# Performance work log

Hardware: AMD Instinct MI355X
Metric: run time of the kernel (lower is better)

The kernel has to match this reference:

```python
import jax, jax.numpy as jnp
import numpy as np

D = 64; H = 6; DH = 32; CB = 16; SB = 8; NSEL = 2; WIN = 7; OUT = 7; HID = 32
SCALE = DH ** -0.5
NEG = -3.4e38  # max_neg_value for fp32 masking


def _rope(x):
    # interleaved (lucidrains rotary-embedding-torch style), theta=10000
    n, d = x.shape[-2], x.shape[-1]
    inv = 1.0 / (10000.0 ** (jnp.arange(0, d, 2, dtype=jnp.float32) / d))
    fr = jnp.arange(n, dtype=jnp.float32)[:, None] * inv[None, :]  # n, d/2
    fr = jnp.repeat(fr, 2, axis=-1)                                # n, d
    c, s = jnp.cos(fr), jnp.sin(fr)
    xr = jnp.stack((-x[..., 1::2], x[..., 0::2]), axis=-1).reshape(x.shape)
    return x * c + xr * s


def reference(x, We, be, gamma, Wq, Wk, Wv, k_pos, v_pos, mem_k, mem_v,
              Wkc1, bkc1, Wkc2, bkc2, Wvc1, bvc1, Wvc2, bvc2,
              Wg, bg, Wo, Wh1, bh1, Wh2, bh2):
    B, N = x.shape
    nC = N // CB  # compressed blocks
    nF = N // SB  # fine/selection blocks

    # per-feature scalar embedding: Linear(1, 64)
    h = x[..., None] * We[0] + be  # B,N,D

    # RMSNorm (F.normalize * sqrt(D) * (gamma + 1))
    nrm = jnp.sqrt(jnp.sum(h * h, axis=-1, keepdims=True))
    hn = h / jnp.maximum(nrm, 1e-12) * jnp.sqrt(float(D)) * (gamma + 1.0)

    def proj(W):
        return jnp.einsum('bnd,de->bne', hn, W).reshape(B, N, H, DH).transpose(0, 2, 1, 3)
    q, k, v = proj(Wq), proj(Wk), proj(Wv)  # B,H,N,DH

    # ---- compressed branch (un-rotated q,k; intra-block pos emb + MLP compressor) ----
    kp = jnp.tile(k_pos, (1, nC, 1))  # H,N,DH
    vp = jnp.tile(v_pos, (1, nC, 1))
    CD = CB * DH
    kc_in = (k + kp).reshape(B, H, nC, CD)
    vc_in = (v + vp).reshape(B, H, nC, CD)
    ck = jax.nn.relu(kc_in @ Wkc1 + bkc1) @ Wkc2 + bkc2  # B,H,nC,DH
    cv = jax.nn.relu(vc_in @ Wvc1 + bvc1) @ Wvc2 + bvc2
    ck = jnp.concatenate([jnp.broadcast_to(mem_k, (B, H, 1, DH)), ck], axis=2)
    cv = jnp.concatenate([jnp.broadcast_to(mem_v, (B, H, 1, DH)), cv], axis=2)
    csim = jnp.einsum('bhid,bhjd->bhij', q, ck) * SCALE  # B,H,N,1+nC
    ck_last = jnp.concatenate([jnp.array([-1]), (jnp.arange(nC) + 1) * CB - 1])
    cmask = ck_last[None, :] < jnp.arange(N)[:, None]    # causal: block fully in past (mem kv always visible)
    csim = jnp.where(cmask, csim, NEG)
    c_out = jnp.einsum('bhij,bhjd->bhid', jax.nn.softmax(csim, axis=-1), cv)

    # ---- importance scores -> top-k selection blocks ----
    # compress_block_size != selection_block_size: repeat compressed scores, block-causal mask,
    # mean-pool to selection granularity (uniform within block -> direct mapping), pad+softmax
    rep = CB // SB
    imp = csim[..., 1:][..., jnp.arange(nF) // rep]  # B,H,N,nF
    qb = jnp.arange(N) // SB
    imp = jnp.where(qb[:, None] > jnp.arange(nF)[None, :], imp, NEG)  # strictly-past blocks only
    imp = jnp.concatenate([jnp.full(imp.shape[:-1] + (1,), -1e3, imp.dtype), imp], axis=-1)
    p = jax.nn.softmax(imp, axis=-1)[..., 1:]
    vals, idx = jax.lax.top_k(p, NSEL)  # B,H,N,NSEL

    # rotary only for fine + sliding branches
    qr, kr = _rope(q), _rope(k)

    # ---- fine (selected-block) branch ----
    sel = jnp.concatenate([idx, jnp.broadcast_to(qb[None, None, :, None], (B, H, N, 1))], axis=-1)  # own block appended
    kb = kr.reshape(B, H, nF, SB, DH)
    vb = v.reshape(B, H, nF, SB, DH)
    bi = jnp.arange(B)[:, None, None, None]
    hi = jnp.arange(H)[None, :, None, None]
    fk = kb[bi, hi, sel].reshape(B, H, N, (NSEL + 1) * SB, DH)
    fv = vb[bi, hi, sel].reshape(B, H, N, (NSEL + 1) * SB, DH)
    fmask_sel = jnp.repeat(vals > 1e-10, SB, axis=-1)                     # B,H,N,NSEL*SB
    own = jnp.arange(SB)[None, :] <= (jnp.arange(N) % SB)[:, None]        # causal within own block
    fmask = jnp.concatenate([fmask_sel, jnp.broadcast_to(own, (B, H, N, SB))], axis=-1)
    fsim = jnp.einsum('bhid,bhijd->bhij', qr, fk) * SCALE
    fsim = jnp.where(fmask, fsim, NEG)
    f_out = jnp.einsum('bhij,bhijd->bhid', jax.nn.softmax(fsim, axis=-1), fv)

    off = jnp.arange(WIN + 1)
    kidx = jnp.arange(N)[:, None] - off[None, :]
    valid = kidx >= 0
    kidx = jnp.maximum(kidx, 0)
    sk = kr[:, :, kidx]
    sv = v[:, :, kidx]
    ssim = jnp.einsum('bhid,bhiwd->bhiw', qr, sk) * SCALE
    ssim = jnp.where(valid, ssim, NEG)
    s_out = jnp.einsum('bhiw,bhiwd->bhid', jax.nn.softmax(ssim, axis=-1), sv)

    # ---- sigmoid-gated strategy combine (order: compressed, fine, sliding) ----
    g = jax.nn.sigmoid(jnp.einsum('bnd,de->bne', hn, Wg) + bg).reshape(B, N, H, 3).transpose(0, 2, 1, 3)
    out = g[..., 0:1] * c_out + g[..., 1:2] * f_out + g[..., 2:3] * s_out  # B,H,N,DH
    out = out.transpose(0, 2, 1, 3).reshape(B, N, H * DH) @ Wo             # B,N,D

    # model head: mean-pool over features, MLP
    pooled = out.mean(axis=1)
    hh = jax.nn.gelu(pooled @ Wh1 + bh1, approximate=False)
    return hh @ Wh2 + bh2


def setup_inputs() -> dict:
    key = jax.random.key(0)
    ks = jax.random.split(key, 20)
    B, N = 32, 512
    CD = CB * DH
    f32 = jnp.float32

    def rn(k, shape, fan_in):
        return jax.random.normal(k, shape, f32) / np.sqrt(fan_in)

    return {
        'x': jax.random.normal(ks[0], (B, N), f32),
        'We': rn(ks[1], (1, D), 1),
        'be': jnp.zeros((D,), f32),
        'gamma': 0.1 * jax.random.normal(ks[2], (D,), f32),
        'Wq': rn(ks[3], (D, H * DH), D),
        'Wk': rn(ks[4], (D, H * DH), D),
        'Wv': rn(ks[5], (D, H * DH), D),
        'k_pos': 0.02 * jax.random.normal(ks[6], (H, CB, DH), f32),
        'v_pos': 0.02 * jax.random.normal(ks[7], (H, CB, DH), f32),
        'mem_k': 0.02 * jax.random.normal(ks[8], (H, 1, DH), f32),
        'mem_v': 0.02 * jax.random.normal(ks[9], (H, 1, DH), f32),
        'Wkc1': rn(ks[10], (CD, CD), CD), 'bkc1': jnp.zeros((CD,), f32),
        'Wkc2': rn(ks[11], (CD, DH), CD), 'bkc2': jnp.zeros((DH,), f32),
        'Wvc1': rn(ks[12], (CD, CD), CD), 'bvc1': jnp.zeros((CD,), f32),
        'Wvc2': rn(ks[13], (CD, DH), CD), 'bvc2': jnp.zeros((DH,), f32),
        'Wg': rn(ks[14], (D, 3 * H), D),
        'bg': jnp.tile(jnp.array([-2.0, -2.0, 2.0], f32), H),
        'Wo': rn(ks[15], (H * DH, D), H * DH),
        'Wh1': rn(ks[16], (D, HID), D), 'bh1': jnp.zeros((HID,), f32),
        'Wh2': rn(ks[17], (HID, OUT), HID), 'bh2': jnp.zeros((OUT,), f32),
    }
```

## Files before the change

### kernel.cpp

```cpp
#include <hip/hip_runtime.h>

typedef unsigned short ushort_t;
typedef __attribute__((ext_vector_type(8))) short bf16x8;
typedef __attribute__((ext_vector_type(4))) float f32x4;

constexpr int N_   = 512;
constexpr int D_   = 64;
constexpr int H_   = 6;
constexpr int DH_  = 32;
constexpr int CB_  = 16;
constexpr int SB_  = 8;
constexpr int HD_  = H_ * DH_;
constexpr int CD_  = CB_ * DH_;
constexpr int nC_  = N_ / CB_;
constexpr int nF_  = N_ / SB_;
constexpr float SCALE_ = 0.17677669529663687f;
constexpr float NEG_ = -3.4e38f;

__device__ __forceinline__ ushort_t f2bf(float x) {
    unsigned u = __float_as_uint(x);
    unsigned r = u + 0x7FFFu + ((u >> 16) & 1u);
    return (ushort_t)(r >> 16);
}

__device__ __forceinline__ size_t frag_addr(int row, int k) {
    return (size_t)(row >> 4) * 8192 + (size_t)(k >> 5) * 512
         + (size_t)((k >> 3) & 3) * 128 + (size_t)(row & 15) * 8 + (k & 7);
}

__global__ __launch_bounds__(256) void k_cvtW(
    const float* __restrict__ Wk1, const float* __restrict__ Wv1,
    ushort_t* __restrict__ wtk_hi, ushort_t* __restrict__ wtk_lo,
    ushort_t* __restrict__ wtv_hi, ushort_t* __restrict__ wtv_lo)
{
    const float* W = blockIdx.z ? Wv1 : Wk1;
    ushort_t* ohi = blockIdx.z ? wtv_hi : wtk_hi;
    ushort_t* olo = blockIdx.z ? wtv_lo : wtk_lo;
    const int k0 = blockIdx.x * 64, j0 = blockIdx.y * 64;
    const int t = threadIdx.x;
    __shared__ float tile[64][65];
    #pragma unroll 4
    for (int i = 0; i < 16; ++i) {
        const int lin = t + i * 256;
        const int kk = lin >> 6, jj = lin & 63;
        tile[kk][jj] = W[(size_t)(k0 + kk) * 512 + j0 + jj];
    }
    __syncthreads();
    #pragma unroll 4
    for (int i = 0; i < 16; ++i) {
        const int lin = t + i * 256;
        const int jj = lin >> 6, kk = lin & 63;
        const float x = tile[kk][jj];
        const ushort_t h = f2bf(x);
        const float hf = __uint_as_float((unsigned)h << 16);
        const size_t fo = frag_addr(j0 + jj, k0 + kk);
        ohi[fo] = h;
        olo[fo] = f2bf(x - hf);
    }
}

__global__ __launch_bounds__(192) void k_embed(
    const float* __restrict__ x, const float* __restrict__ We, const float* __restrict__ be,
    const float* __restrict__ gamma,
    const float* __restrict__ Wq, const float* __restrict__ Wk, const float* __restrict__ Wv,
    const float* __restrict__ kpos, const float* __restrict__ vpos,
    const float* __restrict__ Wg, const float* __restrict__ bg,
    float* __restrict__ q, float* __restrict__ qr, float* __restrict__ kr,
    float* __restrict__ v,
    ushort_t* __restrict__ kin_hi, ushort_t* __restrict__ kin_lo,
    ushort_t* __restrict__ vin_hi, ushort_t* __restrict__ vin_lo,
    float* __restrict__ g)
{
    const int t  = threadIdx.x;
    const int wv = t >> 6;
    const int ln = t & 63;
    const int n00 = blockIdx.x * 16;
    const int b = n00 / N_;
    const int nbase = n00 % N_;

    __shared__ float hn[16][64];

    for (int r = wv; r < 16; r += 3) {
        const int n = nbase + r;
        float xv = x[b * N_ + n];
        float h = fmaf(xv, We[ln], be[ln]);
        float ss = h * h;
        #pragma unroll
        for (int off = 32; off; off >>= 1) ss += __shfl_down(ss, off);
        ss = __shfl(ss, 0);
        float sc = 8.0f / fmaxf(sqrtf(ss), 1e-12f);
        hn[r][ln] = h * sc * (gamma[ln] + 1.0f);
    }
    __syncthreads();

    const int e  = ln + (wv << 6);
    const int hh = e >> 5;
    const int dh = e & 31;
    float aq[16], ak[16], av[16];
    #pragma unroll
    for (int r = 0; r < 16; ++r) { aq[r] = 0.f; ak[r] = 0.f; av[r] = 0.f; }
    for (int dd = 0; dd < 64; dd += 4) {
        float wq4[4], wk4[4], wv4[4];
        #pragma unroll
        for (int u = 0; u < 4; ++u) {
            wq4[u] = Wq[(dd + u) * HD_ + e];
            wk4[u] = Wk[(dd + u) * HD_ + e];
            wv4[u] = Wv[(dd + u) * HD_ + e];
        }
        #pragma unroll
        for (int r = 0; r < 16; ++r) {
            const float4 hv = *(const float4*)&hn[r][dd];
            aq[r] = fmaf(hv.x, wq4[0], aq[r]);
            aq[r] = fmaf(hv.y, wq4[1], aq[r]);
            aq[r] = fmaf(hv.z, wq4[2], aq[r]);
            aq[r] = fmaf(hv.w, wq4[3], aq[r]);
            ak[r] = fmaf(hv.x, wk4[0], ak[r]);
            ak[r] = fmaf(hv.y, wk4[1], ak[r]);
            ak[r] = fmaf(hv.z, wk4[2], ak[r]);
            ak[r] = fmaf(hv.w, wk4[3], ak[r]);
            av[r] = fmaf(hv.x, wv4[0], av[r]);
            av[r] = fmaf(hv.y, wv4[1], av[r]);
            av[r] = fmaf(hv.z, wv4[2], av[r]);
            av[r] = fmaf(hv.w, wv4[3], av[r]);
        }
    }
    const float invf = exp2f((float)(dh & ~1) * -0.41524101186092029f);
    #pragma unroll
    for (int r = 0; r < 16; ++r) {
        const int n = nbase + r;
        const size_t o = ((size_t)(b * H_ + hh) * N_ + n) * DH_ + dh;
        q[o] = aq[r];
        v[o] = av[r];
        const int pix = (hh * CB_ + (n & (CB_ - 1))) * DH_ + dh;
        const float kinv = ak[r] + kpos[pix];
        const float vinv = av[r] + vpos[pix];
        {
            const int row = (b * H_ + hh) * nC_ + (n >> 4);
            const int k   = (n & 15) * 32 + dh;
            const size_t fo = frag_addr(row, k);
            const ushort_t kh = f2bf(kinv);
            kin_hi[fo] = kh;
            kin_lo[fo] = f2bf(kinv - __uint_as_float((unsigned)kh << 16));
            const ushort_t vh = f2bf(vinv);
            vin_hi[fo] = vh;
            vin_lo[fo] = f2bf(vinv - __uint_as_float((unsigned)vh << 16));
        }
        const float aqp = __shfl_xor(aq[r], 1);
        const float akp = __shfl_xor(ak[r], 1);
        float sA, cA;
        __sincosf((float)n * invf, &sA, &cA);
        float rq, rk;
        if (dh & 1) { rq = fmaf(aqp, sA, aq[r] * cA); rk = fmaf(akp, sA, ak[r] * cA); }
        else        { rq = fmaf(-aqp, sA, aq[r] * cA); rk = fmaf(-akp, sA, ak[r] * cA); }
        qr[o] = rq; kr[o] = rk;
    }

    if (ln < 18) {
        for (int r = wv; r < 16; r += 3) {
            const int n = nbase + r;
            float a = bg[ln];
            for (int dd = 0; dd < 64; ++dd) a = fmaf(hn[r][dd], Wg[dd * 18 + ln], a);
            const float gv = 1.0f / (1.0f + __expf(-a));
            g[((size_t)(b * H_ + ln / 3) * N_ + n) * 3 + (ln % 3)] = gv;
        }
    }
}

__global__ __launch_bounds__(256) void k_compress(
    const ushort_t* __restrict__ kin_hi, const ushort_t* __restrict__ kin_lo,
    const ushort_t* __restrict__ vin_hi, const ushort_t* __restrict__ vin_lo,
    const ushort_t* __restrict__ wtk_hi, const ushort_t* __restrict__ wtk_lo,
    const ushort_t* __restrict__ wtv_hi, const ushort_t* __restrict__ wtv_lo,
    const float* __restrict__ bk1, const float* __restrict__ Wk2, const float* __restrict__ bk2,
    const float* __restrict__ bv1, const float* __restrict__ Wv2, const float* __restrict__ bv2,
    const float* __restrict__ mk, const float* __restrict__ mv,
    float* __restrict__ ck, float* __restrict__ cv)
{
    const bool isv = blockIdx.y != 0;
    const ushort_t* xhi = isv ? vin_hi : kin_hi;
    const ushort_t* xlo = isv ? vin_lo : kin_lo;
    const ushort_t* whi = isv ? wtv_hi : wtk_hi;
    const ushort_t* wlo = isv ? wtv_lo : wtk_lo;
    const float* b1 = isv ? bv1 : bk1;
    const float* W2 = isv ? Wv2 : Wk2;
    const float* b2 = isv ? bv2 : bk2;
    const float* mtok = isv ? mv : mk;
    float* outp = isv ? cv : ck;

    const int row0 = blockIdx.x * 32;
    const int t = threadIdx.x;
    const int w = t >> 6, l = t & 63;
    const int lrow = l & 15, kg = l >> 4;
    const int n0w = w * 128;

    __shared__ float hid[32 * 512];
    __shared__ float wred[4 * 16 * 32];

    if (t < 32) {
        outp[(size_t)blockIdx.x * 33 * DH_ + t] = mtok[(blockIdx.x % H_) * DH_ + t];
    }

    f32x4 acc[2][8];
    #pragma unroll
    for (int nt = 0; nt < 8; ++nt) {
        const float bv_ = b1[n0w + nt * 16 + lrow];
        #pragma unroll
        for (int mt = 0; mt < 2; ++mt) {
            acc[mt][nt][0] = bv_; acc[mt][nt][1] = bv_;
            acc[mt][nt][2] = bv_; acc[mt][nt][3] = bv_;
        }
    }
    const ushort_t* Ah = xhi + (size_t)(row0 >> 4) * 8192;
    const ushort_t* Al = xlo + (size_t)(row0 >> 4) * 8192;
    const ushort_t* Bh = whi + (size_t)(n0w >> 4) * 8192;
    const ushort_t* Bl = wlo + (size_t)(n0w >> 4) * 8192;
    const int lofs = l * 8;

    for (int ks = 0; ks < 16; ++ks) {
        const int kb = ks * 512 + lofs;
        const bf16x8 ah0 = *(const bf16x8*)(Ah + kb);
        const bf16x8 ah1 = *(const bf16x8*)(Ah + 8192 + kb);
        const bf16x8 al0 = *(const bf16x8*)(Al + kb);
        const bf16x8 al1 = *(const bf16x8*)(Al + 8192 + kb);
        #pragma unroll
        for (int nt = 0; nt < 8; ++nt) {
            const bf16x8 bh = *(const bf16x8*)(Bh + nt * 8192 + kb);
            const bf16x8 bl = *(const bf16x8*)(Bl + nt * 8192 + kb);
            acc[0][nt] = __builtin_amdgcn_mfma_f32_16x16x32_bf16(ah0, bh, acc[0][nt], 0, 0, 0);
            acc[0][nt] = __builtin_amdgcn_mfma_f32_16x16x32_bf16(ah0, bl, acc[0][nt], 0, 0, 0);
            acc[0][nt] = __builtin_amdgcn_mfma_f32_16x16x32_bf16(al0, bh, acc[0][nt], 0, 0, 0);
            acc[1][nt] = __builtin_amdgcn_mfma_f32_16x16x32_bf16(ah1, bh, acc[1][nt], 0, 0, 0);
            acc[1][nt] = __builtin_amdgcn_mfma_f32_16x16x32_bf16(ah1, bl, acc[1][nt], 0, 0, 0);
            acc[1][nt] = __builtin_amdgcn_mfma_f32_16x16x32_bf16(al1, bh, acc[1][nt], 0, 0, 0);
        }
    }
    #pragma unroll
    for (int mt = 0; mt < 2; ++mt) {
        #pragma unroll
        for (int nt = 0; nt < 8; ++nt) {
            const int col = n0w + nt * 16 + lrow;
            #pragma unroll
            for (int r = 0; r < 4; ++r) {
                const int row = mt * 16 + kg * 4 + r;
                hid[row * 512 + col] = fmaxf(acc[mt][nt][r], 0.0f);
            }
        }
    }
    __syncthreads();

    const int o = t & 31, seg = t >> 5;
    for (int half = 0; half < 2; ++half) {
        const int r0 = half * 16;
        float s[16];
        #pragma unroll
        for (int r = 0; r < 16; ++r) s[r] = 0.f;
        for (int di = 0; di < 64; ++di) {
            const int dd = seg * 64 + di;
            const float w2 = W2[(size_t)dd * 32 + o];
            #pragma unroll
            for (int r = 0; r < 16; ++r) s[r] = fmaf(hid[(r0 + r) * 512 + dd], w2, s[r]);
        }
        #pragma unroll
        for (int r = 0; r < 16; ++r) s[r] += __shfl_xor(s[r], 32);
        if (l < 32) {
            #pragma unroll
            for (int r = 0; r < 16; ++r) wred[(w * 16 + r) * 32 + o] = s[r];
        }
        __syncthreads();
        {
            const int rr = t >> 5;
            #pragma unroll
            for (int u = 0; u < 2; ++u) {
                const int r = rr + u * 8;
                const float val = wred[r * 32 + o] + wred[(16 + r) * 32 + o]
                                + wred[(32 + r) * 32 + o] + wred[(48 + r) * 32 + o] + b2[o];
                const int grow = row0 + r0 + r;
                outp[((size_t)(grow >> 5) * 33 + 1 + (grow & 31)) * DH_ + o] = val;
            }
        }
        __syncthreads();
    }
}

__global__ __launch_bounds__(256) void k_attn(
    const float* __restrict__ q, const float* __restrict__ qr,
    const float* __restrict__ kr, const float* __restrict__ v,
    const float* __restrict__ ck, const float* __restrict__ cv,
    const float* __restrict__ g, float* __restrict__ partial)
{
    const int t = threadIdx.x;
    const int sub = t & 3;
    const int wv = t >> 6;
    const int l = t & 63;
    const int bh = blockIdx.x >> 3;
    const int blk = blockIdx.x & 7;
    const int qi = t >> 2;
    const int n = blk * 64 + qi;
    const int qb = n >> 3;

    float qv[8];
    {
        const float4* p = (const float4*)(q + ((size_t)bh * N_ + n) * DH_ + sub * 8);
        const float4 f0 = p[0], f1 = p[1];
        qv[0]=f0.x; qv[1]=f0.y; qv[2]=f0.z; qv[3]=f0.w;
        qv[4]=f1.x; qv[5]=f1.y; qv[6]=f1.z; qv[7]=f1.w;
    }
    const float* ckb = ck + (size_t)bh * 33 * DH_;
    const float* cvb = cv + (size_t)bh * 33 * DH_;

    float mx = -INFINITY, den = 0.f;
    float cres[8];
    #pragma unroll
    for (int d = 0; d < 8; ++d) cres[d] = 0.f;
    float m2 = -1000.0f, sum2 = 1.0f;
    float v1 = -INFINITY, v2 = -INFINITY;
    int i1 = 0, i2 = 0;

    const int jend = 1 + max(n >> 4, (qb + 1) >> 1);
    for (int j = 0; j < jend; ++j) {
        float a = 0.f;
        {
            const float4* kp = (const float4*)(ckb + j * DH_ + sub * 8);
            const float4 f0 = kp[0], f1 = kp[1];
            a = fmaf(qv[0], f0.x, a); a = fmaf(qv[1], f0.y, a);
            a = fmaf(qv[2], f0.z, a); a = fmaf(qv[3], f0.w, a);
            a = fmaf(qv[4], f1.x, a); a = fmaf(qv[5], f1.y, a);
            a = fmaf(qv[6], f1.z, a); a = fmaf(qv[7], f1.w, a);
        }
        a += __shfl_xor(a, 1);
        a += __shfl_xor(a, 2);
        const bool ok = (j == 0) || (j * CB_ - 1 < n);
        a = ok ? a * SCALE_ : NEG_;

        float p;
        if (a > mx) {
            const float sc_ = __expf(mx - a);
            den *= sc_;
            #pragma unroll
            for (int d = 0; d < 8; ++d) cres[d] *= sc_;
            mx = a; p = 1.0f;
        } else {
            p = __expf(a - mx);
        }
        den += p;
        {
            const float4* vp = (const float4*)(cvb + j * DH_ + sub * 8);
            const float4 f0 = vp[0], f1 = vp[1];
            cres[0] = fmaf(p, f0.x, cres[0]); cres[1] = fmaf(p, f0.y, cres[1]);
            cres[2] = fmaf(p, f0.z, cres[2]); cres[3] = fmaf(p, f0.w, cres[3]);
            cres[4] = fmaf(p, f1.x, cres[4]); cres[5] = fmaf(p, f1.y, cres[5]);
            cres[6] = fmaf(p, f1.z, cres[6]); cres[7] = fmaf(p, f1.w, cres[7]);
        }

        if (j >= 1) {
            const int f0i = 2 * (j - 1);
            const int cnt = (qb > f0i) + (qb > f0i + 1);
            if (cnt) {
                if (a > m2) {
                    sum2 = fmaf(sum2, __expf(m2 - a), (float)cnt);
                    m2 = a;
                } else {
                    sum2 = fmaf((float)cnt, __expf(a - m2), sum2);
                }
                if (a > v1) {
                    if (cnt == 2) { v2 = a; i2 = f0i + 1; }
                    else          { v2 = v1; i2 = i1; }
                    v1 = a; i1 = f0i;
                } else if (a > v2) {
                    v2 = a; i2 = f0i;
                }
            }
        }
    }
    {
        const float invd = 1.0f / den;
        #pragma unroll
        for (int d = 0; d < 8; ++d) cres[d] *= invd;
    }
    const float isum = 1.0f / sum2;
    const bool bm0 = __expf(v1 - m2) * isum > 1e-10f;
    const bool bm1 = __expf(v2 - m2) * isum > 1e-10f;

    float qrv[8];
    {
        const float4* p = (const float4*)(qr + ((size_t)bh * N_ + n) * DH_ + sub * 8);
        const float4 f0 = p[0], f1 = p[1];
        qrv[0]=f0.x; qrv[1]=f0.y; qrv[2]=f0.z; qrv[3]=f0.w;
        qrv[4]=f1.x; qrv[5]=f1.y; qrv[6]=f1.z; qrv[7]=f1.w;
    }
    const float* krb = kr + (size_t)bh * N_ * DH_;
    const float* vb  = v  + (size_t)bh * N_ * DH_;

    int blocks[3]; bool bmask[3];
    blocks[0] = i1; blocks[1] = i2; blocks[2] = qb;
    bmask[0] = bm0; bmask[1] = bm1; bmask[2] = true;

    float fmx = -INFINITY, fden = 0.f;
    float fo[8];
    #pragma unroll
    for (int d = 0; d < 8; ++d) fo[d] = 0.f;
    #pragma unroll
    for (int s = 0; s < 3; ++s) {
        const int base = blocks[s] * SB_;
        #pragma unroll
        for (int j = 0; j < 8; ++j) {
            const int row = base + j;
            float a = 0.f;
            {
                const float4* kp = (const float4*)(krb + (size_t)row * DH_ + sub * 8);
                const float4 f0 = kp[0], f1 = kp[1];
                a = fmaf(qrv[0], f0.x, a); a = fmaf(qrv[1], f0.y, a);
                a = fmaf(qrv[2], f0.z, a); a = fmaf(qrv[3], f0.w, a);
                a = fmaf(qrv[4], f1.x, a); a = fmaf(qrv[5], f1.y, a);
                a = fmaf(qrv[6], f1.z, a); a = fmaf(qrv[7], f1.w, a);
            }
            a += __shfl_xor(a, 1);
            a += __shfl_xor(a, 2);
            const bool ok = (s < 2) ? bmask[s] : (j <= (n & 7));
            a = ok ? a * SCALE_ : NEG_;

            float p;
            if (a > fmx) {
                const float sc_ = __expf(fmx - a);
                fden *= sc_;
                #pragma unroll
                for (int d = 0; d < 8; ++d) fo[d] *= sc_;
                fmx = a; p = 1.0f;
            } else {
                p = __expf(a - fmx);
            }
            fden += p;
            const float4* vp = (const float4*)(vb + (size_t)row * DH_ + sub * 8);
            const float4 f0 = vp[0], f1 = vp[1];
            fo[0] = fmaf(p, f0.x, fo[0]); fo[1] = fmaf(p, f0.y, fo[1]);
            fo[2] = fmaf(p, f0.z, fo[2]); fo[3] = fmaf(p, f0.w, fo[3]);
            fo[4] = fmaf(p, f1.x, fo[4]); fo[5] = fmaf(p, f1.y, fo[5]);
            fo[6] = fmaf(p, f1.z, fo[6]); fo[7] = fmaf(p, f1.w, fo[7]);
        }
    }
    const float finv = 1.0f / fden;

    float wmx = -INFINITY, wden = 0.f;
    float so[8];
    #pragma unroll
    for (int d = 0; d < 8; ++d) so[d] = 0.f;
    #pragma unroll
    for (int w = 0; w < 8; ++w) {
        const int row = (n - w) >= 0 ? (n - w) : 0;
        float a;
        if (w <= n) {
            a = 0.f;
            const float4* kp = (const float4*)(krb + (size_t)row * DH_ + sub * 8);
            const float4 f0 = kp[0], f1 = kp[1];
            a = fmaf(qrv[0], f0.x, a); a = fmaf(qrv[1], f0.y, a);
            a = fmaf(qrv[2], f0.z, a); a = fmaf(qrv[3], f0.w, a);
            a = fmaf(qrv[4], f1.x, a); a = fmaf(qrv[5], f1.y, a);
            a = fmaf(qrv[6], f1.z, a); a = fmaf(qrv[7], f1.w, a);
            a += __shfl_xor(a, 1);
            a += __shfl_xor(a, 2);
            a *= SCALE_;
        } else a = NEG_;

        float p;
        if (a > wmx) {
            const float sc_ = __expf(wmx - a);
            wden *= sc_;
            #pragma unroll
            for (int d = 0; d < 8; ++d) so[d] *= sc_;
            wmx = a; p = 1.0f;
        } else {
            p = __expf(a - wmx);
        }
        wden += p;
        const float4* vp = (const float4*)(vb + (size_t)row * DH_ + sub * 8);
        const float4 f0 = vp[0], f1 = vp[1];
        so[0] = fmaf(p, f0.x, so[0]); so[1] = fmaf(p, f0.y, so[1]);
        so[2] = fmaf(p, f0.z, so[2]); so[3] = fmaf(p, f0.w, so[3]);
        so[4] = fmaf(p, f1.x, so[4]); so[5] = fmaf(p, f1.y, so[5]);
        so[6] = fmaf(p, f1.z, so[6]); so[7] = fmaf(p, f1.w, so[7]);
    }
    const float winv = 1.0f / wden;

    const float g0 = g[((size_t)bh * N_ + n) * 3];
    const float g1 = g[((size_t)bh * N_ + n) * 3 + 1];
    const float g2 = g[((size_t)bh * N_ + n) * 3 + 2];
    float o[8];
    #pragma unroll
    for (int d = 0; d < 8; ++d)
        o[d] = g0 * cres[d] + g1 * (fo[d] * finv) + g2 * (so[d] * winv);

    #pragma unroll
    for (int d = 0; d < 8; ++d) {
        o[d] += __shfl_down(o[d], 32);
        o[d] += __shfl_down(o[d], 16);
        o[d] += __shfl_down(o[d], 8);
        o[d] += __shfl_down(o[d], 4);
    }
    __shared__ float red[4][32];
    if (l < 4) {
        #pragma unroll
        for (int d = 0; d < 8; ++d) red[wv][l * 8 + d] = o[d];
    }
    __syncthreads();
    if (t < 32) {
        const float s = red[0][t] + red[1][t] + red[2][t] + red[3][t];
        partial[((size_t)bh * 8 + blk) * 32 + t] = s;
    }
}

__global__ void k_head(const float* __restrict__ partial, const float* __restrict__ Wo,
                       const float* __restrict__ Wh1, const float* __restrict__ bh1,
                       const float* __restrict__ Wh2, const float* __restrict__ bh2,
                       float* __restrict__ out)
{
    const int b = blockIdx.x;
    const int t = threadIdx.x;
    __shared__ float cs[192];
    __shared__ float pooled[64];
    __shared__ float hid[32];
    for (int i = t; i < 192; i += 64) {
        const int h = i >> 5, dh = i & 31;
        float s = 0.f;
        #pragma unroll
        for (int sg = 0; sg < 8; ++sg)
            s += partial[(((size_t)(b * H_ + h)) * 8 + sg) * 32 + dh];
        cs[i] = s;
    }
    __syncthreads();
    float a = 0.f;
    for (int e = 0; e < 192; ++e) a = fmaf(cs[e], Wo[e * 64 + t], a);
    pooled[t] = a * (1.0f / (float)N_);
    __syncthreads();
    if (t < 32) {
        float s = bh1[t];
        for (int d = 0; d < 64; ++d) s = fmaf(pooled[d], Wh1[d * 32 + t], s);
        hid[t] = 0.5f * s * (1.0f + erff(s * 0.7071067811865476f));
    }
    __syncthreads();
    if (t < 7) {
        float s = bh2[t];
        for (int j = 0; j < 32; ++j) s = fmaf(hid[j], Wh2[j * 7 + t], s);
        out[b * 7 + t] = s;
    }
}

extern "C" void kernel_launch(void* const* d_in, const int* in_sizes, int n_in,
                              void* d_out, int out_size, void* d_ws, size_t ws_size,
                              hipStream_t stream)
{
    const float* x     = (const float*)d_in[0];
    const float* We    = (const float*)d_in[1];
    const float* be    = (const float*)d_in[2];
    const float* gamma = (const float*)d_in[3];
    const float* Wq    = (const float*)d_in[4];
    const float* Wk    = (const float*)d_in[5];
    const float* Wv    = (const float*)d_in[6];
    const float* kpos  = (const float*)d_in[7];
    const float* vpos  = (const float*)d_in[8];
    const float* mk    = (const float*)d_in[9];
    const float* mv    = (const float*)d_in[10];
    const float* Wkc1  = (const float*)d_in[11];
    const float* bkc1  = (const float*)d_in[12];
    const float* Wkc2  = (const float*)d_in[13];
    const float* bkc2  = (const float*)d_in[14];
    const float* Wvc1  = (const float*)d_in[15];
    const float* bvc1  = (const float*)d_in[16];
    const float* Wvc2  = (const float*)d_in[17];
    const float* bvc2  = (const float*)d_in[18];
    const float* Wg    = (const float*)d_in[19];
    const float* bg    = (const float*)d_in[20];
    const float* Wo    = (const float*)d_in[21];
    const float* Wh1   = (const float*)d_in[22];
    const float* bh1   = (const float*)d_in[23];
    const float* Wh2   = (const float*)d_in[24];
    const float* bh2   = (const float*)d_in[25];
    float* out = (float*)d_out;

    const int B = in_sizes[0] / N_;
    const int BH = B * H_;
    const int BHN = BH * N_;
    const size_t SZ = (size_t)BHN * DH_;

    float* ws   = (float*)d_ws;
    float* q_   = ws;
    float* qr_  = ws + SZ;
    float* kr_  = ws + 2 * SZ;
    float* v_   = ws + 3 * SZ;
    ushort_t* kin_hi = (ushort_t*)(ws + 4 * SZ);
    ushort_t* kin_lo = kin_hi + SZ;
    ushort_t* vin_hi = kin_hi + 2 * SZ;
    ushort_t* vin_lo = kin_hi + 3 * SZ;
    float* ck_  = ws + 6 * SZ;
    float* cv_  = ck_ + (size_t)BH * 33 * DH_;
    float* g_   = cv_ + (size_t)BH * 33 * DH_;
    float* partial_ = g_ + (size_t)BHN * 3;
    ushort_t* wtk_hi = (ushort_t*)(partial_ + (size_t)BH * 8 * 32);
    ushort_t* wtk_lo = wtk_hi + 512 * 512;
    ushort_t* wtv_hi = wtk_hi + 2 * 512 * 512;
    ushort_t* wtv_lo = wtk_hi + 3 * 512 * 512;

    k_cvtW<<<dim3(8, 8, 2), dim3(256), 0, stream>>>(
        Wkc1, Wvc1, wtk_hi, wtk_lo, wtv_hi, wtv_lo);
    k_embed<<<dim3(B * N_ / 16), dim3(192), 0, stream>>>(
        x, We, be, gamma, Wq, Wk, Wv, kpos, vpos, Wg, bg,
        q_, qr_, kr_, v_, kin_hi, kin_lo, vin_hi, vin_lo, g_);
    k_compress<<<dim3(BH, 2), dim3(256), 0, stream>>>(
        kin_hi, kin_lo, vin_hi, vin_lo, wtk_hi, wtk_lo, wtv_hi, wtv_lo,
        bkc1, Wkc2, bkc2, bvc1, Wvc2, bvc2, mk, mv, ck_, cv_);
    k_attn<<<dim3(BHN / 64), dim3(256), 0, stream>>>(
        q_, qr_, kr_, v_, ck_, cv_, g_, partial_);
    k_head<<<dim3(B), dim3(64), 0, stream>>>(partial_, Wo, Wh1, bh1, Wh2, bh2, out);
}
```

Baseline: 147.6 us.

## Stage local K/V window and compressed KV in LDS for attention kernel

```diff
diff --git a/kernel.cpp b/kernel.cpp
--- a/kernel.cpp
+++ b/kernel.cpp
@@ -297,6 +297,33 @@
     const int qi = t >> 2;
     const int n = blk * 64 + qi;
     const int qb = n >> 3;
+    const int gbase = blk * 64 - 8;
+
+    __shared__ float krs[72 * 36];
+    __shared__ float vs [72 * 36];
+    __shared__ float cks[33 * 32];
+    __shared__ float cvs[33 * 32];
+    __shared__ float red[4][32];
+
+    const float* krb = kr + (size_t)bh * N_ * DH_;
+    const float* vb  = v  + (size_t)bh * N_ * DH_;
+    {
+        const float4* krg = (const float4*)krb;
+        const float4* vg  = (const float4*)vb;
+        #pragma unroll
+        for (int i = t; i < 72 * 8; i += 256) {
+            const int srow = i >> 3, c4 = i & 7;
+            int grow = gbase + srow;
+            grow = grow < 0 ? 0 : (grow > N_ - 1 ? N_ - 1 : grow);
+            *(float4*)&krs[srow * 36 + c4 * 4] = krg[grow * 8 + c4];
+            *(float4*)&vs [srow * 36 + c4 * 4] = vg[grow * 8 + c4];
+        }
+        if (t < 264) {
+            ((float4*)cks)[t] = ((const float4*)(ck + (size_t)bh * 33 * DH_))[t];
+            ((float4*)cvs)[t] = ((const float4*)(cv + (size_t)bh * 33 * DH_))[t];
+        }
+    }
+    __syncthreads();
 
     float qv[8];
     {
@@ -305,8 +332,6 @@
         qv[0]=f0.x; qv[1]=f0.y; qv[2]=f0.z; qv[3]=f0.w;
         qv[4]=f1.x; qv[5]=f1.y; qv[6]=f1.z; qv[7]=f1.w;
     }
-    const float* ckb = ck + (size_t)bh * 33 * DH_;
-    const float* cvb = cv + (size_t)bh * 33 * DH_;
 
     float mx = -INFINITY, den = 0.f;
     float cres[8];
@@ -320,7 +345,7 @@
     for (int j = 0; j < jend; ++j) {
         float a = 0.f;
         {
-            const float4* kp = (const float4*)(ckb + j * DH_ + sub * 8);
+            const float4* kp = (const float4*)&cks[j * 32 + sub * 8];
             const float4 f0 = kp[0], f1 = kp[1];
             a = fmaf(qv[0], f0.x, a); a = fmaf(qv[1], f0.y, a);
             a = fmaf(qv[2], f0.z, a); a = fmaf(qv[3], f0.w, a);
@@ -344,7 +369,7 @@
         }
         den += p;
         {
-            const float4* vp = (const float4*)(cvb + j * DH_ + sub * 8);
+            const float4* vp = (const float4*)&cvs[j * 32 + sub * 8];
             const float4 f0 = vp[0], f1 = vp[1];
             cres[0] = fmaf(p, f0.x, cres[0]); cres[1] = fmaf(p, f0.y, cres[1]);
             cres[2] = fmaf(p, f0.z, cres[2]); cres[3] = fmaf(p, f0.w, cres[3]);
@@ -388,20 +413,18 @@
         qrv[0]=f0.x; qrv[1]=f0.y; qrv[2]=f0.z; qrv[3]=f0.w;
         qrv[4]=f1.x; qrv[5]=f1.y; qrv[6]=f1.z; qrv[7]=f1.w;
     }
-    const float* krb = kr + (size_t)bh * N_ * DH_;
-    const float* vb  = v  + (size_t)bh * N_ * DH_;
-
-    int blocks[3]; bool bmask[3];
-    blocks[0] = i1; blocks[1] = i2; blocks[2] = qb;
-    bmask[0] = bm0; bmask[1] = bm1; bmask[2] = true;
+
+    int blocks2[2]; bool bmask2[2];
+    blocks2[0] = i1; blocks2[1] = i2;
+    bmask2[0] = bm0; bmask2[1] = bm1;
 
     float fmx = -INFINITY, fden = 0.f;
     float fo[8];
     #pragma unroll
     for (int d = 0; d < 8; ++d) fo[d] = 0.f;
     #pragma unroll
-    for (int s = 0; s < 3; ++s) {
-        const int base = blocks[s] * SB_;
+    for (int s = 0; s < 2; ++s) {
+        const int base = blocks2[s] * SB_;
         #pragma unroll
         for (int j = 0; j < 8; ++j) {
             const int row = base + j;
@@ -416,8 +439,7 @@
             }
             a += __shfl_xor(a, 1);
             a += __shfl_xor(a, 2);
-            const bool ok = (s < 2) ? bmask[s] : (j <= (n & 7));
-            a = ok ? a * SCALE_ : NEG_;
+            a = bmask2[s] ? a * SCALE_ : NEG_;
 
             float p;
             if (a > fmx) {
@@ -438,6 +460,43 @@
             fo[6] = fmaf(p, f1.z, fo[6]); fo[7] = fmaf(p, f1.w, fo[7]);
         }
     }
+    {
+        const int slot0 = qb * 8 - gbase;
+        #pragma unroll
+        for (int j = 0; j < 8; ++j) {
+            const int slot = slot0 + j;
+            float a = 0.f;
+            {
+                const float4* kp = (const float4*)&krs[slot * 36 + sub * 8];
+                const float4 f0 = kp[0], f1 = kp[1];
+                a = fmaf(qrv[0], f0.x, a); a = fmaf(qrv[1], f0.y, a);
+                a = fmaf(qrv[2], f0.z, a); a = fmaf(qrv[3], f0.w, a);
+                a = fmaf(qrv[4], f1.x, a); a = fmaf(qrv[5], f1.y, a);
+                a = fmaf(qrv[6], f1.z, a); a = fmaf(qrv[7], f1.w, a);
+            }
+            a += __shfl_xor(a, 1);
+            a += __shfl_xor(a, 2);
+            a = (j <= (n & 7)) ? a * SCALE_ : NEG_;
+
+            float p;
+            if (a > fmx) {
+                const float sc_ = __expf(fmx - a);
+                fden *= sc_;
+                #pragma unroll
+                for (int d = 0; d < 8; ++d) fo[d] *= sc_;
+                fmx = a; p = 1.0f;
+            } else {
+                p = __expf(a - fmx);
+            }
+            fden += p;
+            const float4* vp = (const float4*)&vs[slot * 36 + sub * 8];
+            const float4 f0 = vp[0], f1 = vp[1];
+            fo[0] = fmaf(p, f0.x, fo[0]); fo[1] = fmaf(p, f0.y, fo[1]);
+            fo[2] = fmaf(p, f0.z, fo[2]); fo[3] = fmaf(p, f0.w, fo[3]);
+            fo[4] = fmaf(p, f1.x, fo[4]); fo[5] = fmaf(p, f1.y, fo[5]);
+            fo[6] = fmaf(p, f1.z, fo[6]); fo[7] = fmaf(p, f1.w, fo[7]);
+        }
+    }
     const float finv = 1.0f / fden;
 
     float wmx = -INFINITY, wden = 0.f;
@@ -447,10 +506,11 @@
     #pragma unroll
     for (int w = 0; w < 8; ++w) {
         const int row = (n - w) >= 0 ? (n - w) : 0;
+        const int slot = row - gbase;
         float a;
         if (w <= n) {
             a = 0.f;
-            const float4* kp = (const float4*)(krb + (size_t)row * DH_ + sub * 8);
+            const float4* kp = (const float4*)&krs[slot * 36 + sub * 8];
             const float4 f0 = kp[0], f1 = kp[1];
             a = fmaf(qrv[0], f0.x, a); a = fmaf(qrv[1], f0.y, a);
             a = fmaf(qrv[2], f0.z, a); a = fmaf(qrv[3], f0.w, a);
@@ -472,7 +532,7 @@
             p = __expf(a - wmx);
         }
         wden += p;
-        const float4* vp = (const float4*)(vb + (size_t)row * DH_ + sub * 8);
+        const float4* vp = (const float4*)&vs[slot * 36 + sub * 8];
         const float4 f0 = vp[0], f1 = vp[1];
         so[0] = fmaf(p, f0.x, so[0]); so[1] = fmaf(p, f0.y, so[1]);
         so[2] = fmaf(p, f0.z, so[2]); so[3] = fmaf(p, f0.w, so[3]);
@@ -496,7 +556,6 @@
         o[d] += __shfl_down(o[d], 8);
         o[d] += __shfl_down(o[d], 4);
     }
-    __shared__ float red[4][32];
     if (l < 4) {
         #pragma unroll
         for (int d = 0; d < 8; ++d) red[wv][l * 8 + d] = o[d];
```

Measured after the change: 150.8 us. +2.1%, slower.
